# Kernel optimization log

Hardware: AMD Instinct MI355X
Metric: run time of the kernel (lower is better)

## Reference

```python
import jax, jax.numpy as jnp
import numpy as np

N_NODES = 100000
D_IN = 128
D_OUT = 128
B, T, S = 8, 4096, 25


def setup_inputs() -> dict:
    key = jax.random.key(0)
    k1, k2, k3 = jax.random.split(key, 3)
    features = jax.random.normal(k1, (N_NODES, D_IN), dtype=jnp.float32)
    sample_res = jax.random.randint(k2, (B, T, S), 0, N_NODES, dtype=jnp.int64)
    # glorot-uniform init for [D_IN, D_OUT]
    limit = np.sqrt(6.0 / (D_IN + D_OUT)).astype(np.float32)
    weights = jax.random.uniform(k3, (D_IN, D_OUT), dtype=jnp.float32,
                                 minval=-limit, maxval=limit)
    return {"features": features, "sample_res": sample_res, "weights": weights}


def reference(features, sample_res, weights):
    # gather neighbor embeddings: [B, T, S, D]
    sampled = features[sample_res]
    # mean over sampled-neighbor axis -> [B, T, D]
    neigh_vecs = jnp.mean(sampled, axis=2)
    # shared linear transform + relu (bias=False per init defaults)
    out = jnp.einsum('btd,do->bto', neigh_vecs, weights)
    return jax.nn.relu(out)
```

## Files before the change

kernel.cpp:

```cpp
#include <hip/hip_runtime.h>


#define DEG 25
#define DIM 128

typedef __attribute__((ext_vector_type(8))) short short8;
typedef __attribute__((ext_vector_type(4))) float floatx4;

__device__ __forceinline__ unsigned short f2bf(float f) {
    unsigned u = __float_as_uint(f);
    return (unsigned short)((u + 0x7fffu + ((u >> 16) & 1u)) >> 16);
}

#define BSTRIDE 136

__global__ __launch_bounds__(256, 2) void gemm_fw(
    const float* __restrict__ A,
    const float* __restrict__ B,
    unsigned short* __restrict__ G,
    int M)
{
    __shared__ unsigned short sBt[DIM * BSTRIDE];

    const int tid = threadIdx.x;

    {
        const float4* B4 = (const float4*)B;
#pragma unroll
        for (int i = 0; i < 16; ++i) {
            const int linear = i * 256 + tid;
            const int k  = linear >> 5;
            const int c4 = linear & 31;
            const float4 v = B4[linear];
            const int n = c4 * 4;
            sBt[(n + 0) * BSTRIDE + k] = f2bf(v.x);
            sBt[(n + 1) * BSTRIDE + k] = f2bf(v.y);
            sBt[(n + 2) * BSTRIDE + k] = f2bf(v.z);
            sBt[(n + 3) * BSTRIDE + k] = f2bf(v.w);
        }
    }
    __syncthreads();

    const int wave = tid >> 6;
    const int lane = tid & 63;
    const int quad = lane >> 4;
    const int l16  = lane & 15;

    const int rw0 = blockIdx.x * 128 + wave * 32;

    floatx4 acc[2][8];
#pragma unroll
    for (int mt = 0; mt < 2; ++mt)
#pragma unroll
        for (int nt = 0; nt < 8; ++nt)
            acc[mt][nt] = (floatx4){0.f, 0.f, 0.f, 0.f};

#pragma unroll
    for (int kt = 0; kt < 4; ++kt) {
        const int k0 = kt * 32;

        short8 afrag[2];
#pragma unroll
        for (int mt = 0; mt < 2; ++mt) {
            int row = rw0 + mt * 16 + l16;
            if (row >= M) row = M - 1;
            const float* ap = A + (size_t)row * DIM + k0 + quad * 8;
            const float4 x = *(const float4*)ap;
            const float4 y = *(const float4*)(ap + 4);
            unsigned p0 = (unsigned)f2bf(x.x) | ((unsigned)f2bf(x.y) << 16);
            unsigned p1 = (unsigned)f2bf(x.z) | ((unsigned)f2bf(x.w) << 16);
            unsigned p2 = (unsigned)f2bf(y.x) | ((unsigned)f2bf(y.y) << 16);
            unsigned p3 = (unsigned)f2bf(y.z) | ((unsigned)f2bf(y.w) << 16);
            uint4 packed = make_uint4(p0, p1, p2, p3);
            afrag[mt] = __builtin_bit_cast(short8, packed);
        }

#pragma unroll
        for (int nt = 0; nt < 8; ++nt) {
            const uint4 u = *(const uint4*)&sBt[(nt * 16 + l16) * BSTRIDE + k0 + quad * 8];
            const short8 bfrag = __builtin_bit_cast(short8, u);
#pragma unroll
            for (int mt = 0; mt < 2; ++mt)
                acc[mt][nt] = __builtin_amdgcn_mfma_f32_16x16x32_bf16(
                    afrag[mt], bfrag, acc[mt][nt], 0, 0, 0);
        }
    }

    uint4* G4 = (uint4*)G;
#pragma unroll
    for (int mt = 0; mt < 2; ++mt)
#pragma unroll
        for (int r = 0; r < 4; ++r) {
            const int row = rw0 + mt * 16 + quad * 4 + r;
            if (row < M) {
                unsigned p0 = (unsigned)f2bf(acc[mt][0][r]) | ((unsigned)f2bf(acc[mt][1][r]) << 16);
                unsigned p1 = (unsigned)f2bf(acc[mt][2][r]) | ((unsigned)f2bf(acc[mt][3][r]) << 16);
                unsigned p2 = (unsigned)f2bf(acc[mt][4][r]) | ((unsigned)f2bf(acc[mt][5][r]) << 16);
                unsigned p3 = (unsigned)f2bf(acc[mt][6][r]) | ((unsigned)f2bf(acc[mt][7][r]) << 16);
                G4[(size_t)row * 16 + l16] = make_uint4(p0, p1, p2, p3);
            }
        }
}

#define GRPB 32

__global__ __launch_bounds__(256, 4) void gather_mean_relu(
    const unsigned short* __restrict__ G,
    const int* __restrict__ idx,
    float* __restrict__ out,
    int n_rows)
{
    __shared__ int sIdx[GRPB * DEG];

    const int tid  = threadIdx.x;
    const int row0 = blockIdx.x * GRPB;

    for (int i = tid; i < GRPB * DEG; i += 256)
        sIdx[i] = idx[(size_t)row0 * DEG + i];
    __syncthreads();

    const int grp = tid >> 4;
    const int l16 = tid & 15;
    const uint4* G4 = (const uint4*)G;

#pragma unroll
    for (int rr = 0; rr < 2; ++rr) {
        const int r = grp + rr * 16;

        uint4 v[DEG];
#pragma unroll
        for (int s = 0; s < DEG; ++s)
            v[s] = G4[(size_t)sIdx[r * DEG + s] * 16 + l16];

        float a0 = 0.f, a1 = 0.f, a2 = 0.f, a3 = 0.f;
        float a4 = 0.f, a5 = 0.f, a6 = 0.f, a7 = 0.f;
#pragma unroll
        for (int s = 0; s < DEG; ++s) {
            a0 += __uint_as_float(v[s].x << 16);
            a1 += __uint_as_float(v[s].x & 0xffff0000u);
            a2 += __uint_as_float(v[s].y << 16);
            a3 += __uint_as_float(v[s].y & 0xffff0000u);
            a4 += __uint_as_float(v[s].z << 16);
            a5 += __uint_as_float(v[s].z & 0xffff0000u);
            a6 += __uint_as_float(v[s].w << 16);
            a7 += __uint_as_float(v[s].w & 0xffff0000u);
        }
        const float inv = 1.0f / 25.0f;
        float* orow = out + (size_t)(row0 + r) * DIM + l16;
        orow[0]   = fmaxf(a0 * inv, 0.f);
        orow[16]  = fmaxf(a1 * inv, 0.f);
        orow[32]  = fmaxf(a2 * inv, 0.f);
        orow[48]  = fmaxf(a3 * inv, 0.f);
        orow[64]  = fmaxf(a4 * inv, 0.f);
        orow[80]  = fmaxf(a5 * inv, 0.f);
        orow[96]  = fmaxf(a6 * inv, 0.f);
        orow[112] = fmaxf(a7 * inv, 0.f);
    }
}

#define RPB 16
#define CG 32

__device__ __forceinline__ float4 relu4(float4 v) {
    return make_float4(fmaxf(v.x, 0.f), fmaxf(v.y, 0.f),
                       fmaxf(v.z, 0.f), fmaxf(v.w, 0.f));
}

__global__ __launch_bounds__(256, 4) void gcn_fused(
    const float* __restrict__ F, const int* __restrict__ idx,
    const float* __restrict__ W, float* __restrict__ out, int n_rows)
{
    __shared__ float4 sV[RPB * CG];
    __shared__ int    sIdx[RPB * DEG];

    const float4* F4 = (const float4*)F;
    const float4* W4 = (const float4*)W;
    float4* out4 = (float4*)out;

    const int tid = threadIdx.x;
    const int row0 = blockIdx.x * RPB;

    for (int i = tid; i < RPB * DEG; i += 256)
        sIdx[i] = idx[(size_t)row0 * DEG + i];
    __syncthreads();

    const int cg = tid & 31;
    const int rs = tid >> 5;

#pragma unroll
    for (int rr = 0; rr < 2; ++rr) {
        const int r = rs + rr * 8;
        int j[DEG];
#pragma unroll
        for (int s = 0; s < DEG; ++s) j[s] = sIdx[r * DEG + s];
        float4 acc = make_float4(0.f, 0.f, 0.f, 0.f);
#pragma unroll
        for (int s = 0; s < DEG; ++s) {
            float4 f = F4[(size_t)j[s] * CG + cg];
            acc.x += f.x; acc.y += f.y; acc.z += f.z; acc.w += f.w;
        }
        const float inv = 1.0f / 25.0f;
        acc.x *= inv; acc.y *= inv; acc.z *= inv; acc.w *= inv;
        sV[r * CG + cg] = acc;
    }
    __syncthreads();

    const float4* vA = &sV[rs * CG];
    const float4* vB = &sV[(rs + 8) * CG];
    float4 o0 = make_float4(0.f, 0.f, 0.f, 0.f);
    float4 o1 = make_float4(0.f, 0.f, 0.f, 0.f);
#pragma unroll 4
    for (int d4 = 0; d4 < CG; ++d4) {
        const float4 a = vA[d4];
        const float4 b = vB[d4];
        const float4 w0 = W4[(size_t)(4 * d4 + 0) * CG + cg];
        const float4 w1 = W4[(size_t)(4 * d4 + 1) * CG + cg];
        const float4 w2 = W4[(size_t)(4 * d4 + 2) * CG + cg];
        const float4 w3 = W4[(size_t)(4 * d4 + 3) * CG + cg];
        o0.x += a.x*w0.x + a.y*w1.x + a.z*w2.x + a.w*w3.x;
        o0.y += a.x*w0.y + a.y*w1.y + a.z*w2.y + a.w*w3.y;
        o0.z += a.x*w0.z + a.y*w1.z + a.z*w2.z + a.w*w3.z;
        o0.w += a.x*w0.w + a.y*w1.w + a.z*w2.w + a.w*w3.w;
        o1.x += b.x*w0.x + b.y*w1.x + b.z*w2.x + b.w*w3.x;
        o1.y += b.x*w0.y + b.y*w1.y + b.z*w2.y + b.w*w3.y;
        o1.z += b.x*w0.z + b.y*w1.z + b.z*w2.z + b.w*w3.z;
        o1.w += b.x*w0.w + b.y*w1.w + b.z*w2.w + b.w*w3.w;
    }
    out4[(size_t)(row0 + rs) * CG + cg]     = relu4(o0);
    out4[(size_t)(row0 + rs + 8) * CG + cg] = relu4(o1);
}

extern "C" void kernel_launch(void* const* d_in, const int* in_sizes, int n_in,
                              void* d_out, int out_size, void* d_ws, size_t ws_size,
                              hipStream_t stream) {
    const float* F   = (const float*)d_in[0];
    const int*   idx = (const int*)d_in[1];
    const float* W   = (const float*)d_in[2];
    float* out = (float*)d_out;

    const int n_nodes = in_sizes[0] / DIM;
    const int n_rows  = in_sizes[1] / DEG;

    const size_t need = (size_t)n_nodes * DIM * sizeof(unsigned short);
    if (ws_size >= need) {
        unsigned short* G = (unsigned short*)d_ws;
        gemm_fw<<<(n_nodes + 127) / 128, 256, 0, stream>>>(F, W, G, n_nodes);
        gather_mean_relu<<<n_rows / GRPB, 256, 0, stream>>>(G, idx, out, n_rows);
    } else {
        gcn_fused<<<n_rows / RPB, 256, 0, stream>>>(F, idx, W, out, n_rows);
    }
}
```

Baseline: 132.0 us.

## Store projected features column-chunked and gather per 16-column chunk for cache locality

The GEMM epilogue now stages bf16 results through shared memory and writes the projected table in a chunked layout: 8 chunks of 16 columns, each chunk contiguous across all nodes, using nontemporal stores. The gather kernel assigns each block one column chunk and 128 output rows. Each lane pair reads 32 bytes per neighbor, so the working set per chunk (about 3.2 MB) can stay cache resident while the index reads repeat eight times. The catch is that indices are reloaded once per chunk and the output is written in 32-byte pieces per row. The fast path now requires the row count to be a multiple of 128.

After: 143.3 us. +8.6%, slower.

```diff
diff --git a/kernel.cpp b/kernel.cpp
--- a/kernel.cpp
+++ b/kernel.cpp
@@ -6,6 +6,7 @@
 
 typedef __attribute__((ext_vector_type(8))) short short8;
 typedef __attribute__((ext_vector_type(4))) float floatx4;
+typedef __attribute__((ext_vector_type(4))) unsigned int uintx4;
 
 __device__ __forceinline__ unsigned short f2bf(float f) {
     unsigned u = __float_as_uint(f);
@@ -71,13 +72,13 @@
             unsigned p1 = (unsigned)f2bf(x.z) | ((unsigned)f2bf(x.w) << 16);
             unsigned p2 = (unsigned)f2bf(y.x) | ((unsigned)f2bf(y.y) << 16);
             unsigned p3 = (unsigned)f2bf(y.z) | ((unsigned)f2bf(y.w) << 16);
-            uint4 packed = make_uint4(p0, p1, p2, p3);
+            uintx4 packed = (uintx4){p0, p1, p2, p3};
             afrag[mt] = __builtin_bit_cast(short8, packed);
         }
 
 #pragma unroll
         for (int nt = 0; nt < 8; ++nt) {
-            const uint4 u = *(const uint4*)&sBt[(nt * 16 + l16) * BSTRIDE + k0 + quad * 8];
+            const uintx4 u = *(const uintx4*)&sBt[(nt * 16 + l16) * BSTRIDE + k0 + quad * 8];
             const short8 bfrag = __builtin_bit_cast(short8, u);
 #pragma unroll
             for (int mt = 0; mt < 2; ++mt)
@@ -86,56 +87,72 @@
         }
     }
 
-    uint4* G4 = (uint4*)G;
-#pragma unroll
-    for (int mt = 0; mt < 2; ++mt)
-#pragma unroll
-        for (int r = 0; r < 4; ++r) {
-            const int row = rw0 + mt * 16 + quad * 4 + r;
-            if (row < M) {
-                unsigned p0 = (unsigned)f2bf(acc[mt][0][r]) | ((unsigned)f2bf(acc[mt][1][r]) << 16);
-                unsigned p1 = (unsigned)f2bf(acc[mt][2][r]) | ((unsigned)f2bf(acc[mt][3][r]) << 16);
-                unsigned p2 = (unsigned)f2bf(acc[mt][4][r]) | ((unsigned)f2bf(acc[mt][5][r]) << 16);
-                unsigned p3 = (unsigned)f2bf(acc[mt][6][r]) | ((unsigned)f2bf(acc[mt][7][r]) << 16);
-                G4[(size_t)row * 16 + l16] = make_uint4(p0, p1, p2, p3);
+    __syncthreads();
+    {
+        unsigned short* sT = sBt + wave * (32 * BSTRIDE);
+#pragma unroll
+        for (int mt = 0; mt < 2; ++mt)
+#pragma unroll
+            for (int nt = 0; nt < 8; ++nt)
+#pragma unroll
+                for (int r = 0; r < 4; ++r)
+                    sT[(mt * 16 + quad * 4 + r) * BSTRIDE + nt * 16 + l16] =
+                        f2bf(acc[mt][nt][r]);
+    }
+    __syncthreads();
+    {
+        const unsigned short* sT = sBt + wave * (32 * BSTRIDE);
+        const int h    = lane & 1;
+        const int nrow = lane >> 1;
+        const int node = rw0 + nrow;
+        if (node < M) {
+            uintx4* G4 = (uintx4*)G;
+#pragma unroll
+            for (int c = 0; c < 8; ++c) {
+                const uintx4 u = *(const uintx4*)&sT[nrow * BSTRIDE + c * 16 + h * 8];
+                __builtin_nontemporal_store(u, &G4[((size_t)c * M + node) * 2 + h]);
             }
         }
-}
-
-#define GRPB 32
-
-__global__ __launch_bounds__(256, 4) void gather_mean_relu(
+    }
+}
+
+#define ROWS_PB 128
+
+__global__ __launch_bounds__(256, 4) void gather_mean_relu_c(
     const unsigned short* __restrict__ G,
     const int* __restrict__ idx,
     float* __restrict__ out,
-    int n_rows)
+    int n_rows, int n_nodes)
 {
-    __shared__ int sIdx[GRPB * DEG];
+    __shared__ int sIdx[ROWS_PB * DEG];
 
     const int tid  = threadIdx.x;
-    const int row0 = blockIdx.x * GRPB;
-
-    for (int i = tid; i < GRPB * DEG; i += 256)
-        sIdx[i] = idx[(size_t)row0 * DEG + i];
-    __syncthreads();
-
-    const int grp = tid >> 4;
-    const int l16 = tid & 15;
-    const uint4* G4 = (const uint4*)G;
-
-#pragma unroll
-    for (int rr = 0; rr < 2; ++rr) {
-        const int r = grp + rr * 16;
-
-        uint4 v[DEG];
-#pragma unroll
-        for (int s = 0; s < DEG; ++s)
-            v[s] = G4[(size_t)sIdx[r * DEG + s] * 16 + l16];
-
-        float a0 = 0.f, a1 = 0.f, a2 = 0.f, a3 = 0.f;
-        float a4 = 0.f, a5 = 0.f, a6 = 0.f, a7 = 0.f;
-#pragma unroll
-        for (int s = 0; s < DEG; ++s) {
+    const int c    = blockIdx.x & 7;
+    const int rb   = blockIdx.x >> 3;
+    const int row0 = rb * ROWS_PB;
+
+    const int* ib = idx + (size_t)row0 * DEG;
+    for (int i = tid; i < ROWS_PB * DEG; i += 256)
+        sIdx[i] = __builtin_nontemporal_load(ib + i);
+    __syncthreads();
+
+    const int h = tid & 1;
+    const int r = tid >> 1;
+    const uintx4* __restrict__ Gc =
+        (const uintx4*)G + (size_t)c * n_nodes * 2 + h;
+
+    float a0 = 0.f, a1 = 0.f, a2 = 0.f, a3 = 0.f;
+    float a4 = 0.f, a5 = 0.f, a6 = 0.f, a7 = 0.f;
+    const int* ip = &sIdx[r * DEG];
+
+#pragma unroll
+    for (int sb = 0; sb < 5; ++sb) {
+        uintx4 v[5];
+#pragma unroll
+        for (int s = 0; s < 5; ++s)
+            v[s] = Gc[(size_t)(unsigned)ip[sb * 5 + s] * 2];
+#pragma unroll
+        for (int s = 0; s < 5; ++s) {
             a0 += __uint_as_float(v[s].x << 16);
             a1 += __uint_as_float(v[s].x & 0xffff0000u);
             a2 += __uint_as_float(v[s].y << 16);
@@ -145,17 +162,16 @@
             a6 += __uint_as_float(v[s].w << 16);
             a7 += __uint_as_float(v[s].w & 0xffff0000u);
         }
-        const float inv = 1.0f / 25.0f;
-        float* orow = out + (size_t)(row0 + r) * DIM + l16;
-        orow[0]   = fmaxf(a0 * inv, 0.f);
-        orow[16]  = fmaxf(a1 * inv, 0.f);
-        orow[32]  = fmaxf(a2 * inv, 0.f);
-        orow[48]  = fmaxf(a3 * inv, 0.f);
-        orow[64]  = fmaxf(a4 * inv, 0.f);
-        orow[80]  = fmaxf(a5 * inv, 0.f);
-        orow[96]  = fmaxf(a6 * inv, 0.f);
-        orow[112] = fmaxf(a7 * inv, 0.f);
-    }
+    }
+
+    const float inv = 1.0f / 25.0f;
+    const floatx4 o0 = (floatx4){fmaxf(a0 * inv, 0.f), fmaxf(a1 * inv, 0.f),
+                                 fmaxf(a2 * inv, 0.f), fmaxf(a3 * inv, 0.f)};
+    const floatx4 o1 = (floatx4){fmaxf(a4 * inv, 0.f), fmaxf(a5 * inv, 0.f),
+                                 fmaxf(a6 * inv, 0.f), fmaxf(a7 * inv, 0.f)};
+    floatx4* op = (floatx4*)(out + (size_t)(row0 + r) * DIM + c * 16 + h * 8);
+    __builtin_nontemporal_store(o0, op);
+    __builtin_nontemporal_store(o1, op + 1);
 }
 
 #define RPB 16
@@ -242,10 +258,11 @@
     const int n_rows  = in_sizes[1] / DEG;
 
     const size_t need = (size_t)n_nodes * DIM * sizeof(unsigned short);
-    if (ws_size >= need) {
+    if (ws_size >= need && (n_rows & (ROWS_PB - 1)) == 0) {
         unsigned short* G = (unsigned short*)d_ws;
         gemm_fw<<<(n_nodes + 127) / 128, 256, 0, stream>>>(F, W, G, n_nodes);
-        gather_mean_relu<<<n_rows / GRPB, 256, 0, stream>>>(G, idx, out, n_rows);
+        gather_mean_relu_c<<<(n_rows / ROWS_PB) * 8, 256, 0, stream>>>(
+            G, idx, out, n_rows, n_nodes);
     } else {
         gcn_fused<<<n_rows / RPB, 256, 0, stream>>>(F, idx, W, out, n_rows);
     }
```
